# Kernel tuning notes

Measured on AMD Instinct MI355X. Metric: run time of the kernel, lower is better.

The kernel has to match this reference:

```python
import jax, jax.numpy as jnp
import numpy as np

B, T, N, D = 64, 10, 64, 4      # batch, time steps, num_vars, input_size
H = 128                          # encoder_hidden
K = 2                            # num_edge_types
EPS = 1e-5                       # BatchNorm eps
_edges = np.ones((N, N)) - np.eye(N)
SEND = jnp.asarray(np.where(_edges)[0])   # [E], E = N*(N-1)
RECV = jnp.asarray(np.where(_edges)[1])   # [E]


def _xavier(key, shape):
    std = (2.0 / (shape[0] + shape[1])) ** 0.5
    return std * jax.random.normal(key, shape, dtype=jnp.float32)


def _mlp(x, w1, b1, w2, b2, g, beta):
    # RefNRIMLP: Linear -> ELU -> (dropout p=0) -> Linear -> ELU -> BatchNorm1d
    h = jax.nn.elu(x @ w1 + b1)
    h = jax.nn.elu(h @ w2 + b2)
    flat = h.reshape(-1, h.shape[-1])  # BN over flattened (batch*objects) axis
    mu = flat.mean(0)
    var = flat.var(0)
    flat = (flat - mu) * jax.lax.rsqrt(var + EPS) * g + beta
    return flat.reshape(h.shape)


def setup_inputs() -> dict:
    key = jax.random.key(0)
    ks = jax.random.split(key, 10)
    inp = {"inputs": jax.random.normal(ks[0], (B, T, N, D), dtype=jnp.float32)}
    fan_ins = {"mlp1": T * D, "mlp2": 2 * H, "mlp3": H, "mlp4": 3 * H}
    for i, (name, nin) in enumerate(fan_ins.items()):
        k1, k2 = jax.random.split(ks[i + 1])
        inp[name + "_w1"] = _xavier(k1, (nin, H))
        inp[name + "_b1"] = jnp.full((H,), 0.1, dtype=jnp.float32)
        inp[name + "_w2"] = _xavier(k2, (H, H))
        inp[name + "_b2"] = jnp.full((H,), 0.1, dtype=jnp.float32)
        inp[name + "_g"] = jnp.ones((H,), dtype=jnp.float32)
        inp[name + "_beta"] = jnp.zeros((H,), dtype=jnp.float32)
    inp["fc_w"] = _xavier(ks[9], (H, K))
    inp["fc_b"] = jnp.full((K,), 0.1, dtype=jnp.float32)
    return inp


def reference(inputs, mlp1_w1, mlp1_b1, mlp1_w2, mlp1_b2, mlp1_g, mlp1_beta,
              mlp2_w1, mlp2_b1, mlp2_w2, mlp2_b2, mlp2_g, mlp2_beta,
              mlp3_w1, mlp3_b1, mlp3_w2, mlp3_b2, mlp3_g, mlp3_beta,
              mlp4_w1, mlp4_b1, mlp4_w2, mlp4_b2, mlp4_g, mlp4_beta,
              fc_w, fc_b):
    # [B,T,N,D] -> [B,N,T*D]
    x = jnp.transpose(inputs, (0, 2, 1, 3)).reshape(B, N, T * D)
    x = _mlp(x, mlp1_w1, mlp1_b1, mlp1_w2, mlp1_b2, mlp1_g, mlp1_beta)
    # node2edge: gather send/recv node embeddings, concat -> [B,E,2H]
    x = jnp.concatenate([x[:, SEND], x[:, RECV]], axis=-1)
    x = _mlp(x, mlp2_w1, mlp2_b1, mlp2_w2, mlp2_b2, mlp2_g, mlp2_beta)
    x_skip = x
    # edge2node: one-hot(recv).T matmul == segment_sum over recv index, then /(N-1)
    agg = jax.ops.segment_sum(jnp.swapaxes(x, 0, 1), RECV, num_segments=N)  # [N,B,H]
    x = jnp.swapaxes(agg, 0, 1) / (N - 1)  # [B,N,H]
    x = _mlp(x, mlp3_w1, mlp3_b1, mlp3_w2, mlp3_b2, mlp3_g, mlp3_beta)
    x = jnp.concatenate([x[:, SEND], x[:, RECV]], axis=-1)  # [B,E,2H]
    x = jnp.concatenate([x, x_skip], axis=-1)  # [B,E,3H]
    x = _mlp(x, mlp4_w1, mlp4_b1, mlp4_w2, mlp4_b2, mlp4_g, mlp4_beta)
    return x @ fc_w + fc_b  # logits [B, E, K]
```

## Files before the change

### kernel.cpp

```cpp
#include <hip/hip_runtime.h>

#define BN_EPS 1e-5f

using h8 = __attribute__((ext_vector_type(8))) _Float16;
using h4v = __attribute__((ext_vector_type(4))) _Float16;
using f4v = __attribute__((ext_vector_type(4))) float;

#define OFF_COEF 0
#define OFF_CVEC 1024
#define OFF_H1 4096
#define OFF_P2 528384
#define OFF_Q2 1052672
#define OFF_H3 1576960
#define OFF_P4 2101248
#define OFF_Q4 2625536
#define OFF_W2P 3149824
#define OFF_W4P 3158016
#define OFF_WCP 3166208
#define OFF_H4B 3174400
#define WS_BYTES 78757888ull

__device__ __forceinline__ float elu_f(float x) {
    return x > 0.f ? x : __expf(x) - 1.f;
}


__device__ __forceinline__ void gemm32_globalW(const float* As, int lda,
                                               const float* __restrict__ Wg, int K,
                                               float acc[2][8], int tx, int ty) {
    const float4* Wg4 = (const float4*)Wg;
#pragma unroll 4
    for (int k = 0; k < K; ++k) {
        float a0 = As[ty * lda + k];
        float a1 = As[(ty + 16) * lda + k];
        float4 wa = Wg4[k * 32 + tx];
        float4 wb = Wg4[k * 32 + 16 + tx];
        const float wv[8] = {wa.x, wa.y, wa.z, wa.w, wb.x, wb.y, wb.z, wb.w};
#pragma unroll
        for (int u = 0; u < 8; ++u) {
            acc[0][u] = fmaf(a0, wv[u], acc[0][u]);
            acc[1][u] = fmaf(a1, wv[u], acc[1][u]);
        }
    }
}

__device__ __forceinline__ void bias_elu32(const float acc[2][8],
                                           const float* __restrict__ bias,
                                           float vals[2][8], int tx) {
    int ca = 4 * tx, cb = 64 + 4 * tx;
    float bv[8] = {bias[ca], bias[ca + 1], bias[ca + 2], bias[ca + 3],
                   bias[cb], bias[cb + 1], bias[cb + 2], bias[cb + 3]};
#pragma unroll
    for (int j = 0; j < 2; ++j)
#pragma unroll
        for (int u = 0; u < 8; ++u)
            vals[j][u] = elu_f(acc[j][u] + bv[u]);
}

__device__ __forceinline__ void store_tile32(float* __restrict__ out, int row0,
                                             const float vals[2][8], int tx, int ty) {
#pragma unroll
    for (int j = 0; j < 2; ++j) {
        int r = row0 + ty + 16 * j;
        *(float4*)(out + r * 128 + 4 * tx) =
            make_float4(vals[j][0], vals[j][1], vals[j][2], vals[j][3]);
        *(float4*)(out + r * 128 + 64 + 4 * tx) =
            make_float4(vals[j][4], vals[j][5], vals[j][6], vals[j][7]);
    }
}

__device__ __forceinline__ void stats_tail32_store(const float vals[2][8], float* red,
                                                   float* __restrict__ slot, int tid,
                                                   int tx, int ty) {
    float ls[8], lq[8];
#pragma unroll
    for (int u = 0; u < 8; ++u) {
        ls[u] = vals[0][u] + vals[1][u];
        lq[u] = vals[0][u] * vals[0][u] + vals[1][u] * vals[1][u];
    }
    __syncthreads();
    int ca = 4 * tx, cb = 64 + 4 * tx;
#pragma unroll
    for (int u = 0; u < 4; ++u) {
        red[ty * 128 + ca + u] = ls[u];
        red[2048 + ty * 128 + ca + u] = lq[u];
        red[ty * 128 + cb + u] = ls[u + 4];
        red[2048 + ty * 128 + cb + u] = lq[u + 4];
    }
    __syncthreads();
    if (tid < 128) {
        float s = 0.f, q = 0.f;
#pragma unroll
        for (int t = 0; t < 16; ++t) {
            s += red[t * 128 + tid];
            q += red[2048 + t * 128 + tid];
        }
        slot[tid] = s;
        slot[128 + tid] = q;
    }
}


__device__ __forceinline__ void gemm2_gw(const _Float16* A0, const _Float16* A1,
                                         const _Float16* __restrict__ wp,
                                         f4v acc0[4][2], f4v acc1[4][2], int lane, int w) {
#pragma unroll
    for (int kc = 0; kc < 4; ++kc) {
        h8 bf0 = *(const h8*)&wp[(((w * 2 + 0) * 4 + kc) * 64 + lane) * 8];
        h8 bf1 = *(const h8*)&wp[(((w * 2 + 1) * 4 + kc) * 64 + lane) * 8];
        h8 af0[4], af1[4];
#pragma unroll
        for (int rt = 0; rt < 4; ++rt) {
            af0[rt] = *(const h8*)&A0[((rt * 4 + kc) * 64 + lane) * 8];
            af1[rt] = *(const h8*)&A1[((rt * 4 + kc) * 64 + lane) * 8];
        }
#pragma unroll
        for (int rt = 0; rt < 4; ++rt) {
            acc0[rt][0] = __builtin_amdgcn_mfma_f32_16x16x32_f16(af0[rt], bf0, acc0[rt][0], 0, 0, 0);
            acc1[rt][0] = __builtin_amdgcn_mfma_f32_16x16x32_f16(af1[rt], bf0, acc1[rt][0], 0, 0, 0);
        }
#pragma unroll
        for (int rt = 0; rt < 4; ++rt) {
            acc0[rt][1] = __builtin_amdgcn_mfma_f32_16x16x32_f16(af0[rt], bf1, acc0[rt][1], 0, 0, 0);
            acc1[rt][1] = __builtin_amdgcn_mfma_f32_16x16x32_f16(af1[rt], bf1, acc1[rt][1], 0, 0, 0);
        }
    }
}

__device__ __forceinline__ void vals_to_afrag(_Float16* Afr, const float vals[4][2][4],
                                              int lane, int w) {
    int cl = lane & 15, quad = lane >> 4;
#pragma unroll
    for (int ctl = 0; ctl < 2; ++ctl) {
        int col = (w * 2 + ctl) * 16 + cl;
        int kc = col >> 5, o = (col >> 3) & 3, j = col & 7;
#pragma unroll
        for (int rt = 0; rt < 4; ++rt)
#pragma unroll
            for (int i = 0; i < 4; ++i) {
                int m = quad * 4 + i;
                Afr[((rt * 4 + kc) * 64 + o * 16 + m) * 8 + j] = (_Float16)vals[rt][ctl][i];
            }
    }
}

__device__ __forceinline__ void stage_pair(_Float16* Afr, const float4* __restrict__ Pr,
                                           const float4* __restrict__ Qr,
                                           const float4* __restrict__ B1, int lane, int kc) {
    int rt = lane >> 4, m = lane & 15;
#pragma unroll
    for (int o = 0; o < 4; ++o) {
        int c4 = kc * 8 + o * 2;
        float4 p0 = Pr[c4], q0 = Qr[c4], bb0 = B1[c4];
        float4 p1 = Pr[c4 + 1], q1 = Qr[c4 + 1], bb1 = B1[c4 + 1];
        h8 v;
        v[0] = (_Float16)elu_f(p0.x + q0.x + bb0.x);
        v[1] = (_Float16)elu_f(p0.y + q0.y + bb0.y);
        v[2] = (_Float16)elu_f(p0.z + q0.z + bb0.z);
        v[3] = (_Float16)elu_f(p0.w + q0.w + bb0.w);
        v[4] = (_Float16)elu_f(p1.x + q1.x + bb1.x);
        v[5] = (_Float16)elu_f(p1.y + q1.y + bb1.y);
        v[6] = (_Float16)elu_f(p1.z + q1.z + bb1.z);
        v[7] = (_Float16)elu_f(p1.w + q1.w + bb1.w);
        *(h8*)&Afr[((rt * 4 + kc) * 64 + o * 16 + m) * 8] = v;
    }
}


__global__ __launch_bounds__(256) void k_mlp1p(const float* __restrict__ x,
                                               const float* __restrict__ w1,
                                               const float* __restrict__ b1,
                                               const float* __restrict__ w2,
                                               const float* __restrict__ b2,
                                               float* __restrict__ h1,
                                               float* __restrict__ slots,
                                               float* __restrict__ sums2,
                                               float* __restrict__ cvec,
                                               const float* __restrict__ w2src,
                                               _Float16* __restrict__ w2p,
                                               const float* __restrict__ w4src,
                                               _Float16* __restrict__ w4p) {
    __shared__ float Xs[32 * 44];
    __shared__ float As[32 * 132];
    int tid = threadIdx.x;
    int blk = blockIdx.x;
    if (blk >= 128) {
        if (blk < 193) {
            int i = (blk - 128) * 256 + tid;
            if (i < 16384) sums2[i] = 0.f;
            else if (i < 16512) cvec[i - 16384] = 0.f;
        } else {
            int second = blk >= 201;
            const float* src = second ? w4src : w2src;
            _Float16* wp = second ? w4p : w2p;
            int flat = (blk - (second ? 201 : 193)) * 256 + tid;
            int g = flat >> 6, L = flat & 63;
            int ct = g >> 2, kc = g & 3;
            int nn = ct * 16 + (L & 15), k0 = kc * 32 + (L >> 4) * 8;
            h8 v;
#pragma unroll
            for (int j = 0; j < 8; ++j) v[j] = (_Float16)src[(k0 + j) * 128 + nn];
            *(h8*)&wp[flat * 8] = v;
        }
        return;
    }
    int tx = tid & 15, ty = tid >> 4;
    int r0 = blk * 32;
    for (int idx = tid; idx < 32 * 40; idx += 256) {
        int r = idx / 40, k = idx - r * 40;
        int rr = r0 + r, b = rr >> 6, n = rr & 63, t = k >> 2, d = k & 3;
        Xs[r * 44 + k] = x[((b * 10 + t) * 64 + n) * 4 + d];
    }
    __syncthreads();
    float acc[2][8] = {};
    gemm32_globalW(Xs, 44, w1, 40, acc, tx, ty);
    float vals[2][8];
    bias_elu32(acc, b1, vals, tx);
    int ca = 4 * tx, cb = 64 + 4 * tx;
#pragma unroll
    for (int j = 0; j < 2; ++j) {
        int r = ty + 16 * j;
#pragma unroll
        for (int u = 0; u < 4; ++u) {
            As[r * 132 + ca + u] = vals[j][u];
            As[r * 132 + cb + u] = vals[j][u + 4];
        }
    }
    __syncthreads();
    float acc2[2][8] = {};
    gemm32_globalW(As, 132, w2, 128, acc2, tx, ty);
    float vals2[2][8];
    bias_elu32(acc2, b2, vals2, tx);
    store_tile32(h1, r0, vals2, tx, ty);
    stats_tail32_store(vals2, As, slots + blk * 256, tid, tx, ty);
}

__global__ __launch_bounds__(256) void k_pqf(const float* __restrict__ h,
                                             const float* __restrict__ slots,
                                             const float* __restrict__ g,
                                             const float* __restrict__ beta,
                                             const float* __restrict__ w,
                                             float* __restrict__ P, float* __restrict__ Q,
                                             float* __restrict__ zero4) {
    __shared__ float Cf[256];
    __shared__ float As[32 * 132];
    int tid = threadIdx.x, tx = tid & 15, ty = tid >> 4;
    int half = blockIdx.x >> 7;
    int r0 = (blockIdx.x & 127) * 32;
    if (zero4 && tid < 64) zero4[blockIdx.x * 64 + tid] = 0.f;
    if (tid < 128) {
        int c = tid;
        float s = 0.f, q = 0.f;
#pragma unroll 8
        for (int t = 0; t < 128; ++t) {
            s += slots[t * 256 + c];
            q += slots[t * 256 + 128 + c];
        }
        float mean = s * (1.f / 4096.f);
        float var = q * (1.f / 4096.f) - mean * mean;
        float a = g[c] * rsqrtf(var + BN_EPS);
        Cf[c] = a;
        Cf[128 + c] = beta[c] - mean * a;
    }
    __syncthreads();
    const float* Wg = w + half * 128 * 128;
    float* out = half ? Q : P;
    const float4* h4p = (const float4*)h;
#pragma unroll
    for (int i = 0; i < 4; ++i) {
        int f4 = tid + i * 256;
        int r = f4 >> 5, c4 = f4 & 31;
        float4 hv = h4p[(r0 + r) * 32 + c4];
        int cb = c4 * 4;
        float4 v;
        v.x = Cf[cb] * hv.x + Cf[128 + cb];
        v.y = Cf[cb + 1] * hv.y + Cf[128 + cb + 1];
        v.z = Cf[cb + 2] * hv.z + Cf[128 + cb + 2];
        v.w = Cf[cb + 3] * hv.w + Cf[128 + cb + 3];
        *(float4*)(As + r * 132 + c4 * 4) = v;
    }
    __syncthreads();
    float acc[2][8] = {};
    gemm32_globalW(As, 132, Wg, 128, acc, tx, ty);
#pragma unroll
    for (int j = 0; j < 2; ++j) {
        int r = r0 + ty + 16 * j;
        *(float4*)(out + r * 128 + 4 * tx) = make_float4(acc[j][0], acc[j][1], acc[j][2], acc[j][3]);
        *(float4*)(out + r * 128 + 64 + 4 * tx) = make_float4(acc[j][4], acc[j][5], acc[j][6], acc[j][7]);
    }
}

__global__ __launch_bounds__(256, 3) void k_mlp2agg(const float* __restrict__ P2,
                                                    const float* __restrict__ Q2,
                                                    const float* __restrict__ b1,
                                                    const _Float16* __restrict__ w2p,
                                                    const float* __restrict__ b2,
                                                    float* __restrict__ aggraw,
                                                    _Float16* __restrict__ h2,
                                                    float* __restrict__ st) {
    __shared__ __align__(16) _Float16 Afr0[9216];
    __shared__ __align__(16) _Float16 Afr1[9216];
    int tid = threadIdx.x;
    int lane = tid & 63, w = tid >> 6, cl = lane & 15, quad = lane >> 4;
    int b = blockIdx.x >> 5, j2 = blockIdx.x & 31;
    int n0 = 2 * j2, n1 = n0 + 1;
    float* stc = st + (blockIdx.x & 63) * 256;
    {
        int r = lane;
        int s0 = (r < 63) ? (r + (r >= n0 ? 1 : 0)) : n0;
        int s1i = (r < 63) ? (r + (r >= n1 ? 1 : 0)) : n1;
        const float4* B1 = (const float4*)b1;
        stage_pair(Afr0, (const float4*)(P2 + (b * 64 + s0) * 128),
                   (const float4*)(Q2 + (b * 64 + n0) * 128), B1, lane, w);
        stage_pair(Afr1, (const float4*)(P2 + (b * 64 + s1i) * 128),
                   (const float4*)(Q2 + (b * 64 + n1) * 128), B1, lane, w);
    }
    __syncthreads();
    f4v acc0[4][2], acc1[4][2];
#pragma unroll
    for (int rt = 0; rt < 4; ++rt)
#pragma unroll
        for (int c = 0; c < 2; ++c) {
            acc0[rt][c] = (f4v){0.f, 0.f, 0.f, 0.f};
            acc1[rt][c] = (f4v){0.f, 0.f, 0.f, 0.f};
        }
    gemm2_gw(Afr0, Afr1, w2p, acc0, acc1, lane, w);
    float v0[2][4][4], v1[2][4][4];
#pragma unroll
    for (int ctl = 0; ctl < 2; ++ctl) {
        int col = (w * 2 + ctl) * 16 + cl;
        float bias = b2[col];
        float a0 = 0.f, a1 = 0.f, sq = 0.f;
#pragma unroll
        for (int rt = 0; rt < 4; ++rt)
#pragma unroll
            for (int i = 0; i < 4; ++i) {
                int row = rt * 16 + quad * 4 + i;
                float va = elu_f(acc0[rt][ctl][i] + bias);
                float vb = elu_f(acc1[rt][ctl][i] + bias);
                if (row == 63) { va = 0.f; vb = 0.f; }
                v0[ctl][rt][i] = va;
                v1[ctl][rt][i] = vb;
                a0 += va;
                a1 += vb;
                sq += va * va + vb * vb;
            }
        a0 += __shfl_xor(a0, 16);
        a1 += __shfl_xor(a1, 16);
        sq += __shfl_xor(sq, 16);
        a0 += __shfl_xor(a0, 32);
        a1 += __shfl_xor(a1, 32);
        sq += __shfl_xor(sq, 32);
        if (quad == 0) {
            aggraw[(b * 64 + n0) * 128 + col] = a0;
            aggraw[(b * 64 + n1) * 128 + col] = a1;
            atomicAdd(stc + col, a0 + a1);
            atomicAdd(stc + 128 + col, sq);
        }
    }
    __syncthreads();
    unsigned short* T0 = (unsigned short*)Afr0;
    unsigned short* T1 = (unsigned short*)Afr1;
#pragma unroll
    for (int ctl = 0; ctl < 2; ++ctl) {
        int col = (w * 2 + ctl) * 16 + cl;
#pragma unroll
        for (int rt = 0; rt < 4; ++rt)
#pragma unroll
            for (int i = 0; i < 4; ++i) {
                int row = rt * 16 + quad * 4 + i;
                _Float16 ha = (_Float16)v0[ctl][rt][i];
                _Float16 hb = (_Float16)v1[ctl][rt][i];
                T0[row * 144 + col] = *(unsigned short*)&ha;
                T1[row * 144 + col] = *(unsigned short*)&hb;
            }
    }
    __syncthreads();
    {
        int rr = tid >> 2, cq = tid & 3;
        if (rr < 63) {
            int s0 = rr + (rr >= n0 ? 1 : 0);
            int e0 = s0 * 63 + (s0 > n0 ? n0 : n0 - 1);
            int s1i = rr + (rr >= n1 ? 1 : 0);
            int e1 = s1i * 63 + (s1i > n1 ? n1 : n1 - 1);
            unsigned short* d0 = (unsigned short*)h2 + ((size_t)b * 4032 + e0) * 128;
            unsigned short* d1 = (unsigned short*)h2 + ((size_t)b * 4032 + e1) * 128;
#pragma unroll
            for (int i = 0; i < 4; ++i) {
                int off = cq * 32 + i * 8;
                *(uint4*)(d0 + off) = *(uint4*)&T0[rr * 144 + off];
                *(uint4*)(d1 + off) = *(uint4*)&T1[rr * 144 + off];
            }
        }
    }
}

__global__ __launch_bounds__(128) void k_wcfin(const float* __restrict__ sums2,
                                               const float* __restrict__ g2,
                                               const float* __restrict__ be2,
                                               const float* __restrict__ w41,
                                               _Float16* __restrict__ wcp,
                                               float* __restrict__ cvec,
                                               float* __restrict__ coef2) {
    __shared__ float red[128];
    __shared__ float pr[2];
    int k = blockIdx.x, c = threadIdx.x;
    red[c] = (c < 64) ? sums2[c * 256 + k] : sums2[(c - 64) * 256 + 128 + k];
    __syncthreads();
    if (c == 0) {
        float s = 0.f, q = 0.f;
#pragma unroll 8
        for (int t = 0; t < 64; ++t) {
            s += red[t];
            q += red[64 + t];
        }
        float mean = s * (1.f / 258048.f);
        float var = q * (1.f / 258048.f) - mean * mean;
        float a = g2[k] * rsqrtf(var + BN_EPS);
        pr[0] = a;
        pr[1] = be2[k] - mean * a;
        coef2[k] = a;
        coef2[128 + k] = pr[1];
    }
    __syncthreads();
    float a2k = pr[0], sh2k = pr[1];
    float wv = w41[(256 + k) * 128 + c];
    int g = (c >> 4) * 4 + (k >> 5);
    int L = ((k >> 3) & 3) * 16 + (c & 15);
    int j = k & 7;
    wcp[(g * 64 + L) * 8 + j] = (_Float16)(a2k * wv);
    atomicAdd(&cvec[c], sh2k * wv);
}

__global__ __launch_bounds__(256) void k_mlp3(const float* __restrict__ raw,
                                              const float* __restrict__ coef2,
                                              const float* __restrict__ w1,
                                              const float* __restrict__ b1,
                                              const float* __restrict__ w2,
                                              const float* __restrict__ b2,
                                              float* __restrict__ h3,
                                              float* __restrict__ slots) {
    __shared__ float As[32 * 132];
    int tid = threadIdx.x, tx = tid & 15, ty = tid >> 4;
    int r0 = blockIdx.x * 32;
    const float4* in4 = (const float4*)raw;
    const float4* av = (const float4*)coef2;
    const float4* cv = (const float4*)(coef2 + 128);
    const float inv63 = 1.f / 63.f;
#pragma unroll
    for (int i = 0; i < 4; ++i) {
        int f4 = tid + i * 256;
        int r = f4 >> 5, c4 = f4 & 31;
        float4 hv = in4[(r0 + r) * 32 + c4];
        float4 a = av[c4], c = cv[c4];
        float4 v;
        v.x = a.x * hv.x * inv63 + c.x;
        v.y = a.y * hv.y * inv63 + c.y;
        v.z = a.z * hv.z * inv63 + c.z;
        v.w = a.w * hv.w * inv63 + c.w;
        *(float4*)(As + r * 132 + c4 * 4) = v;
    }
    __syncthreads();
    float acc[2][8] = {};
    gemm32_globalW(As, 132, w1, 128, acc, tx, ty);
    float vals[2][8];
    bias_elu32(acc, b1, vals, tx);
    __syncthreads();
    int ca = 4 * tx, cb = 64 + 4 * tx;
#pragma unroll
    for (int j = 0; j < 2; ++j) {
        int r = ty + 16 * j;
#pragma unroll
        for (int u = 0; u < 4; ++u) {
            As[r * 132 + ca + u] = vals[j][u];
            As[r * 132 + cb + u] = vals[j][u + 4];
        }
    }
    __syncthreads();
    float acc2[2][8] = {};
    gemm32_globalW(As, 132, w2, 128, acc2, tx, ty);
    float vals2[2][8];
    bias_elu32(acc2, b2, vals2, tx);
    store_tile32(h3, r0, vals2, tx, ty);
    stats_tail32_store(vals2, As, slots + blockIdx.x * 256, tid, tx, ty);
}

__global__ __launch_bounds__(256, 3) void k_mlp4r2(const _Float16* __restrict__ h2,
                                                   const float* __restrict__ P4,
                                                   const float* __restrict__ Q4,
                                                   const _Float16* __restrict__ wcp,
                                                   const float* __restrict__ cvec,
                                                   const float* __restrict__ b1,
                                                   const _Float16* __restrict__ w4p2,
                                                   const float* __restrict__ b2,
                                                   unsigned short* __restrict__ h4,
                                                   float* __restrict__ st) {
    __shared__ __align__(16) _Float16 Afr0[8192];
    __shared__ __align__(16) _Float16 Afr1[8192];
    int tid = threadIdx.x;
    int lane = tid & 63, w = tid >> 6, cl = lane & 15, quad = lane >> 4;
    unsigned t0 = 2u * blockIdx.x, t1 = t0 + 1u;
    unsigned b0 = t0 / 63, b1i = t1 / 63;
    unsigned e00 = (t0 - b0 * 63) * 64, e01 = (t1 - b1i * 63) * 64;
    float* stc = st + (blockIdx.x & 63) * 256;
    {
        const _Float16* hb = h2 + (size_t)t0 * 8192;
#pragma unroll
        for (int j = 0; j < 8; ++j) {
            int win = w * 8 + j;
            int rk = win & 15;
            const _Float16* src = hb + (size_t)((win >> 4) * 64 + (rk >> 2) * 16 + cl) * 128
                                     + (rk & 3) * 32 + quad * 8;
            _Float16* dst = ((win & 16) ? Afr1 : Afr0) + rk * 512;
            __builtin_amdgcn_global_load_lds((const __attribute__((address_space(1))) void*)src,
                                             (__attribute__((address_space(3))) void*)dst,
                                             16, 0, 0);
        }
    }
    __syncthreads();
    f4v acc0[4][2], acc1[4][2];
#pragma unroll
    for (int rt = 0; rt < 4; ++rt)
#pragma unroll
        for (int c = 0; c < 2; ++c) {
            acc0[rt][c] = (f4v){0.f, 0.f, 0.f, 0.f};
            acc1[rt][c] = (f4v){0.f, 0.f, 0.f, 0.f};
        }
    gemm2_gw(Afr0, Afr1, wcp, acc0, acc1, lane, w);
    float v0[4][2][4], v1[4][2][4];
    {
        int col0 = w * 32 + cl, col1 = col0 + 16;
        float base0 = b1[col0] + cvec[col0];
        float base1 = b1[col1] + cvec[col1];
        unsigned sA0 = e00 / 63, sA1 = e01 / 63;
        unsigned baseE0 = sA0 * 63, baseE1 = sA1 * 63;
        unsigned eB0 = baseE0 + 63, eB1 = baseE1 + 63;
        unsigned sB0 = sA0 < 63u ? sA0 + 1u : sA0;
        unsigned sB1 = sA1 < 63u ? sA1 + 1u : sA1;
        const float* PA0 = P4 + (b0 * 64 + sA0) * 128;
        const float* PB0 = P4 + (b0 * 64 + sB0) * 128;
        const float* PA1 = P4 + (b1i * 64 + sA1) * 128;
        const float* PB1 = P4 + (b1i * 64 + sB1) * 128;
        float pA0c0 = PA0[col0], pA0c1 = PA0[col1];
        float pB0c0 = PB0[col0], pB0c1 = PB0[col1];
        float pA1c0 = PA1[col0], pA1c1 = PA1[col1];
        float pB1c0 = PB1[col0], pB1c1 = PB1[col1];
        const float* Qb0 = Q4 + (size_t)b0 * 8192;
        const float* Qb1 = Q4 + (size_t)b1i * 8192;
#pragma unroll
        for (int rt = 0; rt < 4; ++rt)
#pragma unroll
            for (int i = 0; i < 4; ++i) {
                int rr = rt * 16 + quad * 4 + i;
                {
                    unsigned e = e00 + rr;
                    bool hi = e >= eB0;
                    unsigned s = hi ? sB0 : sA0;
                    unsigned jj = e - (hi ? eB0 : baseE0);
                    unsigned rv = jj + (jj >= s ? 1u : 0u);
                    const float* Qr = Qb0 + rv * 128;
                    float p0 = hi ? pB0c0 : pA0c0, p1 = hi ? pB0c1 : pA0c1;
                    v0[rt][0][i] = elu_f(acc0[rt][0][i] + p0 + Qr[col0] + base0);
                    v0[rt][1][i] = elu_f(acc0[rt][1][i] + p1 + Qr[col1] + base1);
                }
                {
                    unsigned e = e01 + rr;
                    bool hi = e >= eB1;
                    unsigned s = hi ? sB1 : sA1;
                    unsigned jj = e - (hi ? eB1 : baseE1);
                    unsigned rv = jj + (jj >= s ? 1u : 0u);
                    const float* Qr = Qb1 + rv * 128;
                    float p0 = hi ? pB1c0 : pA1c0, p1 = hi ? pB1c1 : pA1c1;
                    v1[rt][0][i] = elu_f(acc1[rt][0][i] + p0 + Qr[col0] + base0);
                    v1[rt][1][i] = elu_f(acc1[rt][1][i] + p1 + Qr[col1] + base1);
                }
            }
    }
    __syncthreads();
    vals_to_afrag(Afr0, v0, lane, w);
    vals_to_afrag(Afr1, v1, lane, w);
    __syncthreads();
#pragma unroll
    for (int rt = 0; rt < 4; ++rt)
#pragma unroll
        for (int c = 0; c < 2; ++c) {
            acc0[rt][c] = (f4v){0.f, 0.f, 0.f, 0.f};
            acc1[rt][c] = (f4v){0.f, 0.f, 0.f, 0.f};
        }
    gemm2_gw(Afr0, Afr1, w4p2, acc0, acc1, lane, w);
#pragma unroll
    for (int ctl = 0; ctl < 2; ++ctl) {
        int col = (w * 2 + ctl) * 16 + cl;
        float bias = b2[col];
        float s1 = 0.f, s2 = 0.f;
#pragma unroll
        for (int rt = 0; rt < 4; ++rt)
#pragma unroll
            for (int i = 0; i < 4; ++i) {
                float va = elu_f(acc0[rt][ctl][i] + bias);
                float vb = elu_f(acc1[rt][ctl][i] + bias);
                v0[rt][ctl][i] = va;
                v1[rt][ctl][i] = vb;
                s1 += va + vb;
                s2 += va * va + vb * vb;
            }
        s1 += __shfl_xor(s1, 16);
        s2 += __shfl_xor(s2, 16);
        s1 += __shfl_xor(s1, 32);
        s2 += __shfl_xor(s2, 32);
        if (quad == 0) {
            atomicAdd(stc + col, s1);
            atomicAdd(stc + 128 + col, s2);
        }
    }
    {
        unsigned short* o0 = h4 + (size_t)t0 * 8192;
        unsigned short* o1 = h4 + (size_t)t1 * 8192;
#pragma unroll
        for (int ctl = 0; ctl < 2; ++ctl) {
            int cg = w * 2 + ctl;
#pragma unroll
            for (int rt = 0; rt < 4; ++rt) {
                int idx = ((cg * 4 + rt) * 4 + quad) * 64 + cl * 4;
                h4v a, bvv;
#pragma unroll
                for (int i = 0; i < 4; ++i) {
                    a[i] = (_Float16)v0[rt][ctl][i];
                    bvv[i] = (_Float16)v1[rt][ctl][i];
                }
                *(h4v*)(o0 + idx) = a;
                *(h4v*)(o1 + idx) = bvv;
            }
        }
    }
}

__global__ __launch_bounds__(256) void k_outf(const unsigned short* __restrict__ h4,
                                              const float* __restrict__ sums4,
                                              const float* __restrict__ g4,
                                              const float* __restrict__ be4,
                                              const float* __restrict__ fcw,
                                              const float* __restrict__ fcb,
                                              float* __restrict__ out) {
    __shared__ float U0[128];
    __shared__ float U1[128];
    __shared__ float Cp[4];
    int tid = threadIdx.x;
    if (tid < 128) {
        int c = tid;
        float s = 0.f, q = 0.f;
#pragma unroll 8
        for (int t = 0; t < 64; ++t) {
            s += sums4[t * 256 + c];
            q += sums4[t * 256 + 128 + c];
        }
        float mean = s * (1.f / 258048.f);
        float var = q * (1.f / 258048.f) - mean * mean;
        float a = g4[c] * rsqrtf(var + BN_EPS);
        float sh = be4[c] - mean * a;
        float w0 = fcw[2 * c], w1 = fcw[2 * c + 1];
        U0[c] = a * w0;
        U1[c] = a * w1;
        float p0 = sh * w0, p1 = sh * w1;
#pragma unroll
        for (int off = 1; off < 64; off <<= 1) {
            p0 += __shfl_xor(p0, off);
            p1 += __shfl_xor(p1, off);
        }
        if ((tid & 63) == 0) {
            Cp[(tid >> 6) * 2] = p0;
            Cp[(tid >> 6) * 2 + 1] = p1;
        }
    }
    __syncthreads();
    float C0 = Cp[0] + Cp[2] + fcb[0];
    float C1 = Cp[1] + Cp[3] + fcb[1];
    int lane = tid & 63, w = tid >> 6;
    int quad = lane >> 4, cl = lane & 15;
    float u0r[8], u1r[8];
#pragma unroll
    for (int cg = 0; cg < 8; ++cg) {
        u0r[cg] = U0[cg * 16 + cl];
        u1r[cg] = U1[cg * 16 + cl];
    }
    size_t tile = (size_t)blockIdx.x * 4 + w;
    const unsigned short* hb = h4 + tile * 8192;
#pragma unroll
    for (int rt = 0; rt < 4; ++rt) {
        float s00 = 0.f, s01 = 0.f, s02 = 0.f, s03 = 0.f;
        float s10 = 0.f, s11 = 0.f, s12 = 0.f, s13 = 0.f;
#pragma unroll
        for (int cg = 0; cg < 8; ++cg) {
            h4v hv = *(const h4v*)(hb + ((cg * 4 + rt) * 4 + quad) * 64 + cl * 4);
            float u0 = u0r[cg], u1 = u1r[cg];
            float x0 = (float)hv[0], x1 = (float)hv[1];
            float x2 = (float)hv[2], x3 = (float)hv[3];
            s00 = fmaf(x0, u0, s00); s01 = fmaf(x1, u0, s01);
            s02 = fmaf(x2, u0, s02); s03 = fmaf(x3, u0, s03);
            s10 = fmaf(x0, u1, s10); s11 = fmaf(x1, u1, s11);
            s12 = fmaf(x2, u1, s12); s13 = fmaf(x3, u1, s13);
        }
#pragma unroll
        for (int off = 1; off < 16; off <<= 1) {
            s00 += __shfl_xor(s00, off); s01 += __shfl_xor(s01, off);
            s02 += __shfl_xor(s02, off); s03 += __shfl_xor(s03, off);
            s10 += __shfl_xor(s10, off); s11 += __shfl_xor(s11, off);
            s12 += __shfl_xor(s12, off); s13 += __shfl_xor(s13, off);
        }
        if (cl == 0) {
            size_t R = tile * 64 + rt * 16 + quad * 4;
            *(float4*)(out + R * 2) =
                make_float4(s00 + C0, s10 + C1, s01 + C0, s11 + C1);
            *(float4*)(out + R * 2 + 4) =
                make_float4(s02 + C0, s12 + C1, s03 + C0, s13 + C1);
        }
    }
}


extern "C" void kernel_launch(void* const* d_in, const int* in_sizes, int n_in,
                              void* d_out, int out_size, void* d_ws, size_t ws_size,
                              hipStream_t stream) {
    const float* x = (const float*)d_in[0];
    const float* m1_w1 = (const float*)d_in[1];
    const float* m1_b1 = (const float*)d_in[2];
    const float* m1_w2 = (const float*)d_in[3];
    const float* m1_b2 = (const float*)d_in[4];
    const float* m1_g = (const float*)d_in[5];
    const float* m1_be = (const float*)d_in[6];
    const float* m2_w1 = (const float*)d_in[7];
    const float* m2_b1 = (const float*)d_in[8];
    const float* m2_w2 = (const float*)d_in[9];
    const float* m2_b2 = (const float*)d_in[10];
    const float* m2_g = (const float*)d_in[11];
    const float* m2_be = (const float*)d_in[12];
    const float* m3_w1 = (const float*)d_in[13];
    const float* m3_b1 = (const float*)d_in[14];
    const float* m3_w2 = (const float*)d_in[15];
    const float* m3_b2 = (const float*)d_in[16];
    const float* m3_g = (const float*)d_in[17];
    const float* m3_be = (const float*)d_in[18];
    const float* m4_w1 = (const float*)d_in[19];
    const float* m4_b1 = (const float*)d_in[20];
    const float* m4_w2 = (const float*)d_in[21];
    const float* m4_b2 = (const float*)d_in[22];
    const float* m4_g = (const float*)d_in[23];
    const float* m4_be = (const float*)d_in[24];
    const float* fc_w = (const float*)d_in[25];
    const float* fc_b = (const float*)d_in[26];
    float* out = (float*)d_out;

    float* W = (float*)d_ws;
    float* coef2 = W + OFF_COEF;
    float* cvec = W + OFF_CVEC;
    float* h1 = W + OFF_H1;
    float* aggraw = h1;
    float* sums4 = h1;
    float* P2 = W + OFF_P2;
    float* sums3 = P2;
    float* Q2 = W + OFF_Q2;
    float* h3 = W + OFF_H3;
    float* sums1 = h3;
    float* P4 = W + OFF_P4;
    float* sums2 = P4;
    float* Q4 = W + OFF_Q4;
    _Float16* w2p2 = (_Float16*)(W + OFF_W2P);
    _Float16* w4p2 = (_Float16*)(W + OFF_W4P);
    _Float16* wcp = (_Float16*)(W + OFF_WCP);
    _Float16* h2f = (_Float16*)(W + OFF_H4B);
    unsigned short* h4b = (unsigned short*)(W + OFF_H4B);

    if (ws_size < WS_BYTES) return;

    k_mlp1p<<<209, 256, 0, stream>>>(x, m1_w1, m1_b1, m1_w2, m1_b2, h1, sums1,
                                     sums2, cvec, m2_w2, w2p2, m4_w2, w4p2);
    k_pqf<<<256, 256, 0, stream>>>(h1, sums1, m1_g, m1_be, m2_w1, P2, Q2, nullptr);
    k_mlp2agg<<<2048, 256, 0, stream>>>(P2, Q2, m2_b1, w2p2, m2_b2, aggraw, h2f, sums2);
    k_wcfin<<<128, 128, 0, stream>>>(sums2, m2_g, m2_be, m4_w1, wcp, cvec, coef2);
    k_mlp3<<<128, 256, 0, stream>>>(aggraw, coef2, m3_w1, m3_b1, m3_w2, m3_b2, h3, sums3);
    k_pqf<<<256, 256, 0, stream>>>(h3, sums3, m3_g, m3_be, m4_w1, P4, Q4, sums4);
    k_mlp4r2<<<2016, 256, 0, stream>>>(h2f, P4, Q4, wcp, cvec, m4_b1, w4p2, m4_b2,
                                       h4b, sums4);
    k_outf<<<1008, 256, 0, stream>>>(h4b, sums4, m4_g, m4_be, fc_w, fc_b, out);
}
```

Before: 335.8 us.

## Process one 64-edge tile per block in mlp4 kernel for higher occupancy

The fused mlp4 kernel now handles one 64-row tile per block instead of two. The grid doubles to 4032 blocks and launch bounds rise from 3 to 6 blocks per CU. LDS use and register pressure are halved, aiming for more waves in flight to hide latency. The async global_load_lds prefetch is replaced by plain vector loads that permute into LDS. In exchange, each weight fragment loaded from global is reused across half as many rows, and more atomics hit the stats buffer.

```diff
diff --git a/kernel.cpp b/kernel.cpp
--- a/kernel.cpp
+++ b/kernel.cpp
@@ -123,6 +123,25 @@
         for (int rt = 0; rt < 4; ++rt) {
             acc0[rt][1] = __builtin_amdgcn_mfma_f32_16x16x32_f16(af0[rt], bf1, acc0[rt][1], 0, 0, 0);
             acc1[rt][1] = __builtin_amdgcn_mfma_f32_16x16x32_f16(af1[rt], bf1, acc1[rt][1], 0, 0, 0);
+        }
+    }
+}
+
+__device__ __forceinline__ void gemm1_1t(const _Float16* A,
+                                         const _Float16* __restrict__ wp,
+                                         f4v acc[4][2], int lane, int w) {
+#pragma unroll
+    for (int kc = 0; kc < 4; ++kc) {
+        h8 bf0 = *(const h8*)&wp[(((w * 2 + 0) * 4 + kc) * 64 + lane) * 8];
+        h8 bf1 = *(const h8*)&wp[(((w * 2 + 1) * 4 + kc) * 64 + lane) * 8];
+        h8 af[4];
+#pragma unroll
+        for (int rt = 0; rt < 4; ++rt)
+            af[rt] = *(const h8*)&A[((rt * 4 + kc) * 64 + lane) * 8];
+#pragma unroll
+        for (int rt = 0; rt < 4; ++rt) {
+            acc[rt][0] = __builtin_amdgcn_mfma_f32_16x16x32_f16(af[rt], bf0, acc[rt][0], 0, 0, 0);
+            acc[rt][1] = __builtin_amdgcn_mfma_f32_16x16x32_f16(af[rt], bf1, acc[rt][1], 0, 0, 0);
         }
     }
 }
@@ -485,7 +504,7 @@
     stats_tail32_store(vals2, As, slots + blockIdx.x * 256, tid, tx, ty);
 }
 
-__global__ __launch_bounds__(256, 3) void k_mlp4r2(const _Float16* __restrict__ h2,
+__global__ __launch_bounds__(256, 6) void k_mlp4r3(const _Float16* __restrict__ h2,
                                                    const float* __restrict__ P4,
                                                    const float* __restrict__ Q4,
                                                    const _Float16* __restrict__ wcp,
@@ -495,99 +514,70 @@
                                                    const float* __restrict__ b2,
                                                    unsigned short* __restrict__ h4,
                                                    float* __restrict__ st) {
-    __shared__ __align__(16) _Float16 Afr0[8192];
-    __shared__ __align__(16) _Float16 Afr1[8192];
+    __shared__ __align__(16) _Float16 Afr[8192];
     int tid = threadIdx.x;
     int lane = tid & 63, w = tid >> 6, cl = lane & 15, quad = lane >> 4;
-    unsigned t0 = 2u * blockIdx.x, t1 = t0 + 1u;
-    unsigned b0 = t0 / 63, b1i = t1 / 63;
-    unsigned e00 = (t0 - b0 * 63) * 64, e01 = (t1 - b1i * 63) * 64;
+    unsigned t0 = blockIdx.x;
+    unsigned b0 = t0 / 63;
+    unsigned e00 = (t0 - b0 * 63) * 64;
     float* stc = st + (blockIdx.x & 63) * 256;
     {
         const _Float16* hb = h2 + (size_t)t0 * 8192;
 #pragma unroll
-        for (int j = 0; j < 8; ++j) {
-            int win = w * 8 + j;
-            int rk = win & 15;
-            const _Float16* src = hb + (size_t)((win >> 4) * 64 + (rk >> 2) * 16 + cl) * 128
-                                     + (rk & 3) * 32 + quad * 8;
-            _Float16* dst = ((win & 16) ? Afr1 : Afr0) + rk * 512;
-            __builtin_amdgcn_global_load_lds((const __attribute__((address_space(1))) void*)src,
-                                             (__attribute__((address_space(3))) void*)dst,
-                                             16, 0, 0);
-        }
-    }
-    __syncthreads();
-    f4v acc0[4][2], acc1[4][2];
+        for (int i = 0; i < 4; ++i) {
+            int u = tid + i * 256;
+            int r = u >> 4, cu = u & 15;
+            int g = ((r >> 4) * 4 + (cu >> 2)) * 64 + (cu & 3) * 16 + (r & 15);
+            *(h8*)&Afr[g * 8] = *(const h8*)&hb[r * 128 + cu * 8];
+        }
+    }
+    __syncthreads();
+    f4v acc[4][2];
 #pragma unroll
     for (int rt = 0; rt < 4; ++rt)
 #pragma unroll
-        for (int c = 0; c < 2; ++c) {
-            acc0[rt][c] = (f4v){0.f, 0.f, 0.f, 0.f};
-            acc1[rt][c] = (f4v){0.f, 0.f, 0.f, 0.f};
-        }
-    gemm2_gw(Afr0, Afr1, wcp, acc0, acc1, lane, w);
-    float v0[4][2][4], v1[4][2][4];
+        for (int c = 0; c < 2; ++c)
+            acc[rt][c] = (f4v){0.f, 0.f, 0.f, 0.f};
+    gemm1_1t(Afr, wcp, acc, lane, w);
+    float v0[4][2][4];
     {
         int col0 = w * 32 + cl, col1 = col0 + 16;
         float base0 = b1[col0] + cvec[col0];
         float base1 = b1[col1] + cvec[col1];
-        unsigned sA0 = e00 / 63, sA1 = e01 / 63;
-        unsigned baseE0 = sA0 * 63, baseE1 = sA1 * 63;
-        unsigned eB0 = baseE0 + 63, eB1 = baseE1 + 63;
+        unsigned sA0 = e00 / 63;
+        unsigned baseE0 = sA0 * 63;
+        unsigned eB0 = baseE0 + 63;
         unsigned sB0 = sA0 < 63u ? sA0 + 1u : sA0;
-        unsigned sB1 = sA1 < 63u ? sA1 + 1u : sA1;
         const float* PA0 = P4 + (b0 * 64 + sA0) * 128;
         const float* PB0 = P4 + (b0 * 64 + sB0) * 128;
-        const float* PA1 = P4 + (b1i * 64 + sA1) * 128;
-        const float* PB1 = P4 + (b1i * 64 + sB1) * 128;
         float pA0c0 = PA0[col0], pA0c1 = PA0[col1];
         float pB0c0 = PB0[col0], pB0c1 = PB0[col1];
-        float pA1c0 = PA1[col0], pA1c1 = PA1[col1];
-        float pB1c0 = PB1[col0], pB1c1 = PB1[col1];
         const float* Qb0 = Q4 + (size_t)b0 * 8192;
-        const float* Qb1 = Q4 + (size_t)b1i * 8192;
 #pragma unroll
         for (int rt = 0; rt < 4; ++rt)
 #pragma unroll
             for (int i = 0; i < 4; ++i) {
                 int rr = rt * 16 + quad * 4 + i;
-                {
-                    unsigned e = e00 + rr;
-                    bool hi = e >= eB0;
-                    unsigned s = hi ? sB0 : sA0;
-                    unsigned jj = e - (hi ? eB0 : baseE0);
-                    unsigned rv = jj + (jj >= s ? 1u : 0u);
-                    const float* Qr = Qb0 + rv * 128;
-                    float p0 = hi ? pB0c0 : pA0c0, p1 = hi ? pB0c1 : pA0c1;
-                    v0[rt][0][i] = elu_f(acc0[rt][0][i] + p0 + Qr[col0] + base0);
-                    v0[rt][1][i] = elu_f(acc0[rt][1][i] + p1 + Qr[col1] + base1);
-                }
-                {
-                    unsigned e = e01 + rr;
-                    bool hi = e >= eB1;
-                    unsigned s = hi ? sB1 : sA1;
-                    unsigned jj = e - (hi ? eB1 : baseE1);
-                    unsigned rv = jj + (jj >= s ? 1u : 0u);
-                    const float* Qr = Qb1 + rv * 128;
-                    float p0 = hi ? pB1c0 : pA1c0, p1 = hi ? pB1c1 : pA1c1;
-                    v1[rt][0][i] = elu_f(acc1[rt][0][i] + p0 + Qr[col0] + base0);
-                    v1[rt][1][i] = elu_f(acc1[rt][1][i] + p1 + Qr[col1] + base1);
-                }
+                unsigned e = e00 + rr;
+                bool hi = e >= eB0;
+                unsigned s = hi ? sB0 : sA0;
+                unsigned jj = e - (hi ? eB0 : baseE0);
+                unsigned rv = jj + (jj >= s ? 1u : 0u);
+                const float* Qr = Qb0 + rv * 128;
+                float p0 = hi ? pB0c0 : pA0c0, p1 = hi ? pB0c1 : pA0c1;
+                v0[rt][0][i] = elu_f(acc[rt][0][i] + p0 + Qr[col0] + base0);
+                v0[rt][1][i] = elu_f(acc[rt][1][i] + p1 + Qr[col1] + base1);
             }
     }
     __syncthreads();
-    vals_to_afrag(Afr0, v0, lane, w);
-    vals_to_afrag(Afr1, v1, lane, w);
+    vals_to_afrag(Afr, v0, lane, w);
     __syncthreads();
 #pragma unroll
     for (int rt = 0; rt < 4; ++rt)
 #pragma unroll
-        for (int c = 0; c < 2; ++c) {
-            acc0[rt][c] = (f4v){0.f, 0.f, 0.f, 0.f};
-            acc1[rt][c] = (f4v){0.f, 0.f, 0.f, 0.f};
-        }
-    gemm2_gw(Afr0, Afr1, w4p2, acc0, acc1, lane, w);
+        for (int c = 0; c < 2; ++c)
+            acc[rt][c] = (f4v){0.f, 0.f, 0.f, 0.f};
+    gemm1_1t(Afr, w4p2, acc, lane, w);
 #pragma unroll
     for (int ctl = 0; ctl < 2; ++ctl) {
         int col = (w * 2 + ctl) * 16 + cl;
@@ -597,12 +587,10 @@
         for (int rt = 0; rt < 4; ++rt)
 #pragma unroll
             for (int i = 0; i < 4; ++i) {
-                float va = elu_f(acc0[rt][ctl][i] + bias);
-                float vb = elu_f(acc1[rt][ctl][i] + bias);
+                float va = elu_f(acc[rt][ctl][i] + bias);
                 v0[rt][ctl][i] = va;
-                v1[rt][ctl][i] = vb;
-                s1 += va + vb;
-                s2 += va * va + vb * vb;
+                s1 += va;
+                s2 += va * va;
             }
         s1 += __shfl_xor(s1, 16);
         s2 += __shfl_xor(s2, 16);
@@ -615,21 +603,16 @@
     }
     {
         unsigned short* o0 = h4 + (size_t)t0 * 8192;
-        unsigned short* o1 = h4 + (size_t)t1 * 8192;
 #pragma unroll
         for (int ctl = 0; ctl < 2; ++ctl) {
             int cg = w * 2 + ctl;
 #pragma unroll
             for (int rt = 0; rt < 4; ++rt) {
                 int idx = ((cg * 4 + rt) * 4 + quad) * 64 + cl * 4;
-                h4v a, bvv;
-#pragma unroll
-                for (int i = 0; i < 4; ++i) {
-                    a[i] = (_Float16)v0[rt][ctl][i];
-                    bvv[i] = (_Float16)v1[rt][ctl][i];
-                }
+                h4v a;
+#pragma unroll
+                for (int i = 0; i < 4; ++i) a[i] = (_Float16)v0[rt][ctl][i];
                 *(h4v*)(o0 + idx) = a;
-                *(h4v*)(o1 + idx) = bvv;
             }
         }
     }
@@ -779,7 +762,7 @@
     k_wcfin<<<128, 128, 0, stream>>>(sums2, m2_g, m2_be, m4_w1, wcp, cvec, coef2);
     k_mlp3<<<128, 256, 0, stream>>>(aggraw, coef2, m3_w1, m3_b1, m3_w2, m3_b2, h3, sums3);
     k_pqf<<<256, 256, 0, stream>>>(h3, sums3, m3_g, m3_be, m4_w1, P4, Q4, sums4);
-    k_mlp4r2<<<2016, 256, 0, stream>>>(h2f, P4, Q4, wcp, cvec, m4_b1, w4p2, m4_b2,
+    k_mlp4r3<<<4032, 256, 0, stream>>>(h2f, P4, Q4, wcp, cvec, m4_b1, w4p2, m4_b2,
                                        h4b, sums4);
     k_outf<<<1008, 256, 0, stream>>>(h4b, sums4, m4_g, m4_be, fc_w, fc_b, out);
 }
```

After: 325.1 us. 1.03x faster.
